# Kernel optimization log

Measured on AMD Instinct MI355X. Metric: run time of the kernel, lower is better.

Reference implementation:

```python
import jax, jax.numpy as jnp
import numpy as np

C = 1536          # interim_dim
D2 = 2 * C        # 3072, fc_nlb dim
LN_EPS = 1e-5


def setup_inputs() -> dict:
    key = jax.random.key(0)
    ks = jax.random.split(key, 24)
    B, L = 32, 1024
    s = 0.02
    inp = {
        "x": jax.random.normal(ks[0], (B, C), dtype=jnp.float32),
        "lfb_feats": jax.random.normal(ks[1], (B, L, C), dtype=jnp.float32),
        # 1x1 Conv1d weights act as (C_out, C_in) matmuls
        "theta_w": jax.random.normal(ks[2], (C, C), dtype=jnp.float32) * s,
        "theta_b": jnp.zeros((C,), dtype=jnp.float32),
        "phi_w": jax.random.normal(ks[3], (C, C), dtype=jnp.float32) * s,
        "phi_b": jnp.zeros((C,), dtype=jnp.float32),
        "gi_w": jax.random.normal(ks[4], (C, C), dtype=jnp.float32) * s,
        "gi_b": jnp.zeros((C,), dtype=jnp.float32),
        "ln_g": jnp.ones((C,), dtype=jnp.float32),
        "ln_b": jnp.zeros((C,), dtype=jnp.float32),
        "fc_w": jax.random.normal(ks[5], (C, C), dtype=jnp.float32) * s,
        "fc_b": jnp.zeros((C,), dtype=jnp.float32),
        "fc_nlb_w": jax.random.normal(ks[6], (D2, D2), dtype=jnp.float32) * s,
        "fc_nlb_b": jnp.zeros((D2,), dtype=jnp.float32),
        "fc1_w": jax.random.normal(ks[7], (1, 1024), dtype=jnp.float32) * s,
        "fc1_b": jnp.zeros((1,), dtype=jnp.float32),
        "fc2_w": jax.random.normal(ks[8], (1, 1024), dtype=jnp.float32) * s,
        "fc2_b": jnp.zeros((1,), dtype=jnp.float32),
        "fc3_w": jax.random.normal(ks[9], (1, 1024), dtype=jnp.float32) * s,
        "fc3_b": jnp.zeros((1,), dtype=jnp.float32),
        "fct_w": jax.random.normal(ks[10], (1, D2), dtype=jnp.float32) * s,
        "fct_b": jnp.zeros((1,), dtype=jnp.float32),
    }
    return inp


def _layernorm(x, g, b):
    mu = jnp.mean(x, axis=-1, keepdims=True)
    var = jnp.mean(jnp.square(x - mu), axis=-1, keepdims=True)
    return (x - mu) * jax.lax.rsqrt(var + LN_EPS) * g + b


def reference(x, lfb_feats, theta_w, theta_b, phi_w, phi_b, gi_w, gi_b,
              ln_g, ln_b, fc_w, fc_b, fc_nlb_w, fc_nlb_b,
              fc1_w, fc1_b, fc2_w, fc2_b, fc3_w, fc3_b, fct_w, fct_b):
    # --- _NLBlock on feats = x.unsqueeze(1): query sequence length is 1 ---
    # note: scale = 1/sqrt(1/C) = sqrt(C) (as in the original code)
    scale = jnp.sqrt(jnp.asarray(C, dtype=x.dtype))
    theta = x @ theta_w.T + theta_b                       # (B, C)
    phi = lfb_feats @ phi_w.T + phi_b                     # (B, L, C)
    gi = lfb_feats @ gi_w.T + gi_b                        # (B, L, C)
    scores = jnp.einsum('bc,blc->bl', theta, phi) * scale  # (B, L)
    attn = jax.nn.softmax(scores, axis=-1)
    o = jnp.einsum('bl,blc->bc', attn, gi)                # (B, C)
    o = jax.nn.relu(_layernorm(o, ln_g, ln_b))
    o = o @ fc_w.T + fc_b                                 # dropout -> identity (eval)
    longterm = o + x                                      # residual, (B, C)

    # --- head ---
    feats = jnp.concatenate([x, longterm], axis=1)        # (B, 2C)
    feats = jax.nn.relu(feats @ fc_nlb_w.T + fc_nlb_b)    # dropout -> identity
    f1 = feats[:, :1024]
    f2 = feats[:, 1024:2048]
    f3 = feats[:, 2048:3072]
    p1 = f1 @ fc1_w.T + fc1_b
    p2 = f2 @ fc2_w.T + fc2_b
    p3 = f3 @ fc3_w.T + fc3_b
    pt = feats @ fct_w.T + fct_b
    return jnp.concatenate([p1, p2, p3, pt], axis=1)      # (B, 4)
```

## Files before the change

kernel.cpp:

```cpp
#include <hip/hip_runtime.h>
#include <math.h>

#define B 32
#define C 1536
#define D2 3072
#define L 1024
#define KC 256
#define XPAD 260
#define CH 16
#define LPW 16

__device__ inline float dot4(float4 a, float4 b) {
    return a.x * b.x + a.y * b.y + a.z * b.z + a.w * b.w;
}

__global__ __launch_bounds__(256) void copy_x_k(const float* __restrict__ x,
                                                float* __restrict__ feats) {
    int i = blockIdx.x * 256 + threadIdx.x;
    int b = i / C, j = i % C;
    feats[b * D2 + j] = x[i];
}

__global__ __launch_bounds__(256) void transpose_k(const float* __restrict__ src,
                                                   float* __restrict__ dst, int n) {
    __shared__ float tile[32][33];
    int bx = blockIdx.x * 32, by = blockIdx.y * 32;
    int tx = threadIdx.x & 31, ty0 = threadIdx.x >> 5;
    #pragma unroll
    for (int r = 0; r < 4; ++r) {
        int ty = ty0 + r * 8;
        tile[ty][tx] = src[(size_t)(by + ty) * n + bx + tx];
    }
    __syncthreads();
    #pragma unroll
    for (int r = 0; r < 4; ++r) {
        int ty = ty0 + r * 8;
        dst[(size_t)(bx + ty) * n + by + tx] = tile[tx][ty];
    }
}

__global__ __launch_bounds__(256) void gemm32_splitk(const float* __restrict__ A,
                                                     const float* __restrict__ W,
                                                     float* __restrict__ part,
                                                     int N, int K) {
    __shared__ float xs[32 * XPAD];
    __shared__ float wsm[32 * XPAD];
    int tid = threadIdx.x;
    int j0 = blockIdx.x * 32;
    int kb = blockIdx.y;
    int k0 = kb * KC;

    #pragma unroll
    for (int r = 0; r < 8; ++r) {
        int f = tid + 256 * r;
        int b = f >> 6, kq = f & 63;
        float4 v = *(const float4*)(A + (size_t)b * K + k0 + 4 * kq);
        *(float4*)(xs + b * XPAD + 4 * kq) = v;
    }
    #pragma unroll
    for (int r = 0; r < 8; ++r) {
        int f = tid + 256 * r;
        int j = f >> 6, kq = f & 63;
        float4 v = *(const float4*)(W + (size_t)(j0 + j) * K + k0 + 4 * kq);
        *(float4*)(wsm + j * XPAD + 4 * kq) = v;
    }
    __syncthreads();

    int bb = (tid & 15) * 2;
    int jj = (tid >> 4) * 2;
    const float* x0 = xs + bb * XPAD;
    const float* x1 = xs + (bb + 1) * XPAD;
    const float* w0 = wsm + jj * XPAD;
    const float* w1 = wsm + (jj + 1) * XPAD;
    float a00 = 0.f, a01 = 0.f, a10 = 0.f, a11 = 0.f;
    #pragma unroll 8
    for (int k = 0; k < KC; k += 4) {
        float4 xa = *(const float4*)(x0 + k);
        float4 xb = *(const float4*)(x1 + k);
        float4 wa = *(const float4*)(w0 + k);
        float4 wb = *(const float4*)(w1 + k);
        a00 += dot4(xa, wa); a01 += dot4(xa, wb);
        a10 += dot4(xb, wa); a11 += dot4(xb, wb);
    }
    float* p = part + (size_t)kb * 32 * N;
    p[(size_t)bb * N + j0 + jj]           = a00;
    p[(size_t)bb * N + j0 + jj + 1]       = a01;
    p[(size_t)(bb + 1) * N + j0 + jj]     = a10;
    p[(size_t)(bb + 1) * N + j0 + jj + 1] = a11;
}

__global__ __launch_bounds__(256) void reduce_part(const float* __restrict__ part,
                                                   const float* __restrict__ bias,
                                                   const float* __restrict__ addx,
                                                   float* __restrict__ out,
                                                   float* __restrict__ feats,
                                                   int N, int ksplit, int mode) {
    int i = blockIdx.x * 256 + threadIdx.x;
    int b = i / N, j = i % N;
    float s = 0.f;
    for (int kk = 0; kk < ksplit; ++kk) s += part[(size_t)kk * 32 * N + i];
    if (bias) s += bias[j];
    if (mode == 2) {
        feats[(size_t)b * D2 + C + j] = s + addx[(size_t)b * C + j];
    } else if (mode == 3) {
        out[i] = fmaxf(s, 0.f);
    } else {
        out[i] = s;
    }
}

__global__ __launch_bounds__(256) void flash_k(const float* __restrict__ u,
                                               const float* __restrict__ lfb,
                                               float* __restrict__ pm,
                                               float* __restrict__ ps,
                                               float* __restrict__ pv) {
    int chunk = blockIdx.x;
    int b = blockIdx.y;
    int wave = threadIdx.x >> 6;
    int lane = threadIdx.x & 63;
    int widx = chunk * 4 + wave;

    const float scale = 39.19183588453085f;

    float uu[24];
    const float* ub = u + (size_t)b * C;
    #pragma unroll
    for (int t = 0; t < 6; ++t)
        *(float4*)(uu + 4 * t) = *(const float4*)(ub + 4 * lane + 256 * t);

    float m = -INFINITY, s = 0.f;
    float vv[24];
    #pragma unroll
    for (int t = 0; t < 24; ++t) vv[t] = 0.f;

    int l0 = chunk * (L / CH) + wave;
    for (int i = 0; i < LPW; ++i) {
        int l = l0 + i * 4;
        const float* row = lfb + ((size_t)b * L + l) * C;
        float xx[24];
        #pragma unroll
        for (int t = 0; t < 6; ++t)
            *(float4*)(xx + 4 * t) = *(const float4*)(row + 4 * lane + 256 * t);
        float d = 0.f;
        #pragma unroll
        for (int t = 0; t < 24; ++t) d += xx[t] * uu[t];
        #pragma unroll
        for (int off = 32; off > 0; off >>= 1) d += __shfl_xor(d, off, 64);
        float score = d * scale;
        float mn = fmaxf(m, score);
        float alpha = __expf(m - mn);
        float p = __expf(score - mn);
        s = s * alpha + p;
        #pragma unroll
        for (int t = 0; t < 24; ++t) vv[t] = vv[t] * alpha + p * xx[t];
        m = mn;
    }

    if (lane == 0) { pm[b * 64 + widx] = m; ps[b * 64 + widx] = s; }
    float* pvb = pv + ((size_t)b * 64 + widx) * C;
    #pragma unroll
    for (int t = 0; t < 6; ++t)
        *(float4*)(pvb + 4 * lane + 256 * t) = *(const float4*)(vv + 4 * t);
}

__global__ __launch_bounds__(256) void combine_k(const float* __restrict__ pm,
                                                 const float* __restrict__ ps,
                                                 const float* __restrict__ pv,
                                                 float* __restrict__ v) {
    int b = blockIdx.x;
    int tid = threadIdx.x;
    __shared__ float coef[64];
    if (tid < 64) {
        float mj = pm[b * 64 + tid];
        float M = mj;
        #pragma unroll
        for (int off = 32; off > 0; off >>= 1) M = fmaxf(M, __shfl_xor(M, off, 64));
        float ej = expf(mj - M);
        float S = ps[b * 64 + tid] * ej;
        #pragma unroll
        for (int off = 32; off > 0; off >>= 1) S += __shfl_xor(S, off, 64);
        coef[tid] = ej / S;
    }
    __syncthreads();
    for (int c = tid; c < C; c += 256) {
        float acc = 0.f;
        #pragma unroll 8
        for (int j = 0; j < 64; ++j)
            acc += coef[j] * pv[((size_t)b * 64 + j) * C + c];
        v[(size_t)b * C + c] = acc;
    }
}

__global__ __launch_bounds__(256) void ln_relu_k(const float* __restrict__ o,
                                                 const float* __restrict__ g,
                                                 const float* __restrict__ bt,
                                                 float* __restrict__ out) {
    int b = blockIdx.x, tid = threadIdx.x;
    __shared__ float r1[4], r2[4];
    const float* ob = o + (size_t)b * C;
    float lv[6];
    float s1 = 0.f, s2 = 0.f;
    #pragma unroll
    for (int t = 0; t < 6; ++t) {
        float x = ob[tid + 256 * t];
        lv[t] = x; s1 += x; s2 += x * x;
    }
    #pragma unroll
    for (int off = 32; off > 0; off >>= 1) {
        s1 += __shfl_xor(s1, off, 64);
        s2 += __shfl_xor(s2, off, 64);
    }
    int wave = tid >> 6, lane = tid & 63;
    if (lane == 0) { r1[wave] = s1; r2[wave] = s2; }
    __syncthreads();
    s1 = r1[0] + r1[1] + r1[2] + r1[3];
    s2 = r2[0] + r2[1] + r2[2] + r2[3];
    float mu = s1 / (float)C;
    float var = s2 / (float)C - mu * mu;
    float rstd = 1.0f / sqrtf(var + 1e-5f);
    #pragma unroll
    for (int t = 0; t < 6; ++t) {
        int c = tid + 256 * t;
        float y = (lv[t] - mu) * rstd * g[c] + bt[c];
        out[(size_t)b * C + c] = fmaxf(y, 0.f);
    }
}

__global__ __launch_bounds__(256) void heads_k(const float* __restrict__ h,
                                               const float* __restrict__ w1, const float* __restrict__ b1,
                                               const float* __restrict__ w2, const float* __restrict__ b2,
                                               const float* __restrict__ w3, const float* __restrict__ b3,
                                               const float* __restrict__ wt, const float* __restrict__ bt,
                                               float* __restrict__ out) {
    int b = blockIdx.x;
    int wave = threadIdx.x >> 6, lane = threadIdx.x & 63;
    const float* hb = h + (size_t)b * D2;
    float acc = 0.f;
    if (wave < 3) {
        const float* w = (wave == 0) ? w1 : ((wave == 1) ? w2 : w3);
        const float* hh = hb + wave * 1024;
        #pragma unroll
        for (int t = 0; t < 16; ++t) acc += hh[lane + 64 * t] * w[lane + 64 * t];
    } else {
        #pragma unroll
        for (int t = 0; t < 48; ++t) acc += hb[lane + 64 * t] * wt[lane + 64 * t];
    }
    #pragma unroll
    for (int off = 32; off > 0; off >>= 1) acc += __shfl_xor(acc, off, 64);
    if (lane == 0) {
        float bias = (wave == 0) ? b1[0] : (wave == 1) ? b2[0] : (wave == 2) ? b3[0] : bt[0];
        out[b * 4 + wave] = acc + bias;
    }
}

extern "C" void kernel_launch(void* const* d_in, const int* in_sizes, int n_in,
                              void* d_out, int out_size, void* d_ws, size_t ws_size,
                              hipStream_t stream) {
    (void)in_sizes; (void)n_in; (void)out_size; (void)ws_size;
    const float* x       = (const float*)d_in[0];
    const float* lfb     = (const float*)d_in[1];
    const float* theta_w = (const float*)d_in[2];
    const float* theta_b = (const float*)d_in[3];
    const float* phi_w   = (const float*)d_in[4];
    const float* gi_w    = (const float*)d_in[6];
    const float* gi_b    = (const float*)d_in[7];
    const float* ln_g    = (const float*)d_in[8];
    const float* ln_b    = (const float*)d_in[9];
    const float* fc_w    = (const float*)d_in[10];
    const float* fc_b    = (const float*)d_in[11];
    const float* fcn_w   = (const float*)d_in[12];
    const float* fcn_b   = (const float*)d_in[13];
    const float* w1 = (const float*)d_in[14]; const float* b1 = (const float*)d_in[15];
    const float* w2 = (const float*)d_in[16]; const float* b2 = (const float*)d_in[17];
    const float* w3 = (const float*)d_in[18]; const float* b3 = (const float*)d_in[19];
    const float* wt = (const float*)d_in[20]; const float* bt = (const float*)d_in[21];
    float* out = (float*)d_out;
    float* w = (float*)d_ws;

    float* theta = w;
    float* u     = w + 49152;
    float* part  = w + 98304;
    float* phiT  = w + 1277952;
    float* pm    = w + 98304;
    float* ps    = w + 100352;
    float* pv    = w + 102400;
    float* vbuf  = w + 3637248;
    float* obuf  = w + 3686400;
    float* oln   = w + 3735552;
    float* feats = w + 3784704;
    float* h     = w + 3883008;

    copy_x_k<<<192, 256, 0, stream>>>(x, feats);
    transpose_k<<<dim3(48, 48), 256, 0, stream>>>(phi_w, phiT, C);

    gemm32_splitk<<<dim3(48, 6), 256, 0, stream>>>(x, theta_w, part, C, C);
    reduce_part<<<192, 256, 0, stream>>>(part, theta_b, nullptr, theta, nullptr, C, 6, 0);

    gemm32_splitk<<<dim3(48, 6), 256, 0, stream>>>(theta, phiT, part, C, C);
    reduce_part<<<192, 256, 0, stream>>>(part, nullptr, nullptr, u, nullptr, C, 6, 0);

    flash_k<<<dim3(CH, B), 256, 0, stream>>>(u, lfb, pm, ps, pv);
    combine_k<<<B, 256, 0, stream>>>(pm, ps, pv, vbuf);

    gemm32_splitk<<<dim3(48, 6), 256, 0, stream>>>(vbuf, gi_w, part, C, C);
    reduce_part<<<192, 256, 0, stream>>>(part, gi_b, nullptr, obuf, nullptr, C, 6, 0);

    ln_relu_k<<<B, 256, 0, stream>>>(obuf, ln_g, ln_b, oln);

    gemm32_splitk<<<dim3(48, 6), 256, 0, stream>>>(oln, fc_w, part, C, C);
    reduce_part<<<192, 256, 0, stream>>>(part, fc_b, x, nullptr, feats, C, 6, 2);

    gemm32_splitk<<<dim3(96, 12), 256, 0, stream>>>(feats, fcn_w, part, D2, D2);
    reduce_part<<<384, 256, 0, stream>>>(part, fcn_b, nullptr, h, nullptr, D2, 12, 3);

    heads_k<<<B, 256, 0, stream>>>(h, w1, b1, w2, b2, w3, b3, wt, bt, out);
}
```

Before: 473.5 us.

## Retile skinny GEMMs with 4x4 register tiles, swizzled LDS, and fused reductions

Replaces the split-K GEMM with a 32x128 tile kernel that computes a 4x4 register tile per thread, stages K in chunks of 64 through XOR-swizzled shared memory, and loops over two K chunks per block. Grids and reduction split counts change to match. The x copy is folded into the residual reduce, the gi reduce is fused with LayerNorm/ReLU, and combine_k is split across column blocks for more parallelism. Together these aim to cut launch count, raise arithmetic intensity per LDS load, and improve occupancy for the memory-bound combine. The cost is more partial sums for the reduce kernels to read.

```diff
diff --git a/kernel.cpp b/kernel.cpp
--- a/kernel.cpp
+++ b/kernel.cpp
@@ -5,8 +5,8 @@
 #define C 1536
 #define D2 3072
 #define L 1024
-#define KC 256
-#define XPAD 260
+#define KC 64
+#define KQ 16
 #define CH 16
 #define LPW 16
 
@@ -14,11 +14,8 @@
     return a.x * b.x + a.y * b.y + a.z * b.z + a.w * b.w;
 }
 
-__global__ __launch_bounds__(256) void copy_x_k(const float* __restrict__ x,
-                                                float* __restrict__ feats) {
-    int i = blockIdx.x * 256 + threadIdx.x;
-    int b = i / C, j = i % C;
-    feats[b * D2 + j] = x[i];
+__device__ inline int sw(int row, int q) {
+    return row * KC + ((q ^ ((row >> 2) & 7)) << 2);
 }
 
 __global__ __launch_bounds__(256) void transpose_k(const float* __restrict__ src,
@@ -39,54 +36,61 @@
     }
 }
 
-__global__ __launch_bounds__(256) void gemm32_splitk(const float* __restrict__ A,
-                                                     const float* __restrict__ W,
-                                                     float* __restrict__ part,
-                                                     int N, int K) {
-    __shared__ float xs[32 * XPAD];
-    __shared__ float wsm[32 * XPAD];
+__global__ __launch_bounds__(256) void gemm32t4(const float* __restrict__ A,
+                                                const float* __restrict__ W,
+                                                float* __restrict__ part,
+                                                int N, int K, int kchunks) {
+    __shared__ float xs[32 * KC];
+    __shared__ float wsm[128 * KC];
     int tid = threadIdx.x;
-    int j0 = blockIdx.x * 32;
+    int j0 = blockIdx.x * 128;
     int kb = blockIdx.y;
-    int k0 = kb * KC;
-
-    #pragma unroll
-    for (int r = 0; r < 8; ++r) {
-        int f = tid + 256 * r;
-        int b = f >> 6, kq = f & 63;
-        float4 v = *(const float4*)(A + (size_t)b * K + k0 + 4 * kq);
-        *(float4*)(xs + b * XPAD + 4 * kq) = v;
-    }
-    #pragma unroll
-    for (int r = 0; r < 8; ++r) {
-        int f = tid + 256 * r;
-        int j = f >> 6, kq = f & 63;
-        float4 v = *(const float4*)(W + (size_t)(j0 + j) * K + k0 + 4 * kq);
-        *(float4*)(wsm + j * XPAD + 4 * kq) = v;
-    }
-    __syncthreads();
-
-    int bb = (tid & 15) * 2;
-    int jj = (tid >> 4) * 2;
-    const float* x0 = xs + bb * XPAD;
-    const float* x1 = xs + (bb + 1) * XPAD;
-    const float* w0 = wsm + jj * XPAD;
-    const float* w1 = wsm + (jj + 1) * XPAD;
-    float a00 = 0.f, a01 = 0.f, a10 = 0.f, a11 = 0.f;
-    #pragma unroll 8
-    for (int k = 0; k < KC; k += 4) {
-        float4 xa = *(const float4*)(x0 + k);
-        float4 xb = *(const float4*)(x1 + k);
-        float4 wa = *(const float4*)(w0 + k);
-        float4 wb = *(const float4*)(w1 + k);
-        a00 += dot4(xa, wa); a01 += dot4(xa, wb);
-        a10 += dot4(xb, wa); a11 += dot4(xb, wb);
-    }
-    float* p = part + (size_t)kb * 32 * N;
-    p[(size_t)bb * N + j0 + jj]           = a00;
-    p[(size_t)bb * N + j0 + jj + 1]       = a01;
-    p[(size_t)(bb + 1) * N + j0 + jj]     = a10;
-    p[(size_t)(bb + 1) * N + j0 + jj + 1] = a11;
+    int tb = tid & 7;
+    int tj = tid >> 3;
+
+    float4 acc[4];
+    #pragma unroll
+    for (int r = 0; r < 4; ++r) acc[r] = make_float4(0.f, 0.f, 0.f, 0.f);
+
+    for (int c = 0; c < kchunks; ++c) {
+        int k0 = (kb * kchunks + c) * KC;
+        __syncthreads();
+        #pragma unroll
+        for (int p = 0; p < 2; ++p) {
+            int f = tid + 256 * p;
+            int row = f >> 4, q = f & 15;
+            float4 v = *(const float4*)(A + (size_t)row * K + k0 + 4 * q);
+            *(float4*)(xs + sw(row, q)) = v;
+        }
+        #pragma unroll
+        for (int p = 0; p < 8; ++p) {
+            int f = tid + 256 * p;
+            int row = f >> 4, q = f & 15;
+            float4 v = *(const float4*)(W + (size_t)(j0 + row) * K + k0 + 4 * q);
+            *(float4*)(wsm + sw(row, q)) = v;
+        }
+        __syncthreads();
+        #pragma unroll
+        for (int kq = 0; kq < KQ; ++kq) {
+            float4 xq[4], wq[4];
+            #pragma unroll
+            for (int r = 0; r < 4; ++r) {
+                xq[r] = *(const float4*)(xs + sw(4 * tb + r, kq));
+                wq[r] = *(const float4*)(wsm + sw(4 * tj + r, kq));
+            }
+            #pragma unroll
+            for (int r = 0; r < 4; ++r) {
+                acc[r].x += dot4(xq[r], wq[0]);
+                acc[r].y += dot4(xq[r], wq[1]);
+                acc[r].z += dot4(xq[r], wq[2]);
+                acc[r].w += dot4(xq[r], wq[3]);
+            }
+        }
+    }
+    #pragma unroll
+    for (int r = 0; r < 4; ++r) {
+        *(float4*)(part + ((size_t)kb * 32 + 4 * tb + r) * N + j0 + 4 * tj) = acc[r];
+    }
 }
 
 __global__ __launch_bounds__(256) void reduce_part(const float* __restrict__ part,
@@ -98,14 +102,55 @@
     int i = blockIdx.x * 256 + threadIdx.x;
     int b = i / N, j = i % N;
     float s = 0.f;
-    for (int kk = 0; kk < ksplit; ++kk) s += part[(size_t)kk * 32 * N + i];
+    for (int kk = 0; kk < ksplit; ++kk) s += part[((size_t)kk * 32 + b) * N + j];
     if (bias) s += bias[j];
     if (mode == 2) {
-        feats[(size_t)b * D2 + C + j] = s + addx[(size_t)b * C + j];
+        float xv = addx[i];
+        feats[(size_t)b * D2 + j] = xv;
+        feats[(size_t)b * D2 + C + j] = s + xv;
     } else if (mode == 3) {
         out[i] = fmaxf(s, 0.f);
     } else {
         out[i] = s;
+    }
+}
+
+__global__ __launch_bounds__(256) void reduce_ln_relu(const float* __restrict__ part,
+                                                      const float* __restrict__ bias,
+                                                      const float* __restrict__ g,
+                                                      const float* __restrict__ bt,
+                                                      float* __restrict__ out,
+                                                      int ksplit) {
+    int b = blockIdx.x, tid = threadIdx.x;
+    __shared__ float r1[4], r2[4];
+    float lv[6];
+    float s1 = 0.f, s2 = 0.f;
+    #pragma unroll
+    for (int t = 0; t < 6; ++t) {
+        int c = tid + 256 * t;
+        float acc = 0.f;
+        for (int kk = 0; kk < ksplit; ++kk) acc += part[((size_t)kk * 32 + b) * C + c];
+        acc += bias[c];
+        lv[t] = acc; s1 += acc; s2 += acc * acc;
+    }
+    #pragma unroll
+    for (int off = 32; off > 0; off >>= 1) {
+        s1 += __shfl_xor(s1, off, 64);
+        s2 += __shfl_xor(s2, off, 64);
+    }
+    int wave = tid >> 6, lane = tid & 63;
+    if (lane == 0) { r1[wave] = s1; r2[wave] = s2; }
+    __syncthreads();
+    s1 = r1[0] + r1[1] + r1[2] + r1[3];
+    s2 = r2[0] + r2[1] + r2[2] + r2[3];
+    float mu = s1 / (float)C;
+    float var = s2 / (float)C - mu * mu;
+    float rstd = 1.0f / sqrtf(var + 1e-5f);
+    #pragma unroll
+    for (int t = 0; t < 6; ++t) {
+        int c = tid + 256 * t;
+        float y = (lv[t] - mu) * rstd * g[c] + bt[c];
+        out[(size_t)b * C + c] = fmaxf(y, 0.f);
     }
 }
 
@@ -167,7 +212,8 @@
                                                  const float* __restrict__ ps,
                                                  const float* __restrict__ pv,
                                                  float* __restrict__ v) {
-    int b = blockIdx.x;
+    int cc = blockIdx.x;
+    int b = blockIdx.y;
     int tid = threadIdx.x;
     __shared__ float coef[64];
     if (tid < 64) {
@@ -182,48 +228,12 @@
         coef[tid] = ej / S;
     }
     __syncthreads();
-    for (int c = tid; c < C; c += 256) {
-        float acc = 0.f;
-        #pragma unroll 8
-        for (int j = 0; j < 64; ++j)
-            acc += coef[j] * pv[((size_t)b * 64 + j) * C + c];
-        v[(size_t)b * C + c] = acc;
-    }
-}
-
-__global__ __launch_bounds__(256) void ln_relu_k(const float* __restrict__ o,
-                                                 const float* __restrict__ g,
-                                                 const float* __restrict__ bt,
-                                                 float* __restrict__ out) {
-    int b = blockIdx.x, tid = threadIdx.x;
-    __shared__ float r1[4], r2[4];
-    const float* ob = o + (size_t)b * C;
-    float lv[6];
-    float s1 = 0.f, s2 = 0.f;
-    #pragma unroll
-    for (int t = 0; t < 6; ++t) {
-        float x = ob[tid + 256 * t];
-        lv[t] = x; s1 += x; s2 += x * x;
-    }
-    #pragma unroll
-    for (int off = 32; off > 0; off >>= 1) {
-        s1 += __shfl_xor(s1, off, 64);
-        s2 += __shfl_xor(s2, off, 64);
-    }
-    int wave = tid >> 6, lane = tid & 63;
-    if (lane == 0) { r1[wave] = s1; r2[wave] = s2; }
-    __syncthreads();
-    s1 = r1[0] + r1[1] + r1[2] + r1[3];
-    s2 = r2[0] + r2[1] + r2[2] + r2[3];
-    float mu = s1 / (float)C;
-    float var = s2 / (float)C - mu * mu;
-    float rstd = 1.0f / sqrtf(var + 1e-5f);
-    #pragma unroll
-    for (int t = 0; t < 6; ++t) {
-        int c = tid + 256 * t;
-        float y = (lv[t] - mu) * rstd * g[c] + bt[c];
-        out[(size_t)b * C + c] = fmaxf(y, 0.f);
-    }
+    int c = cc * 256 + tid;
+    float acc = 0.f;
+    #pragma unroll 8
+    for (int j = 0; j < 64; ++j)
+        acc += coef[j] * pv[((size_t)b * 64 + j) * C + c];
+    v[(size_t)b * C + c] = acc;
 }
 
 __global__ __launch_bounds__(256) void heads_k(const float* __restrict__ h,
@@ -277,41 +287,37 @@
     float* out = (float*)d_out;
     float* w = (float*)d_ws;
 
-    float* theta = w;
-    float* u     = w + 49152;
-    float* part  = w + 98304;
-    float* phiT  = w + 1277952;
-    float* pm    = w + 98304;
-    float* ps    = w + 100352;
-    float* pv    = w + 102400;
-    float* vbuf  = w + 3637248;
-    float* obuf  = w + 3686400;
-    float* oln   = w + 3735552;
-    float* feats = w + 3784704;
-    float* h     = w + 3883008;
-
-    copy_x_k<<<192, 256, 0, stream>>>(x, feats);
+    float* phiT  = w;
+    float* part  = w + 2359296;
+    float* pv    = w + 4718592;
+    float* pm    = w + 7864320;
+    float* ps    = w + 7866368;
+    float* theta = w + 7868416;
+    float* u     = w + 7917568;
+    float* vbuf  = w + 7966720;
+    float* oln   = w + 8015872;
+    float* feats = w + 8065024;
+    float* h     = w + 8163328;
+
     transpose_k<<<dim3(48, 48), 256, 0, stream>>>(phi_w, phiT, C);
 
-    gemm32_splitk<<<dim3(48, 6), 256, 0, stream>>>(x, theta_w, part, C, C);
-    reduce_part<<<192, 256, 0, stream>>>(part, theta_b, nullptr, theta, nullptr, C, 6, 0);
-
-    gemm32_splitk<<<dim3(48, 6), 256, 0, stream>>>(theta, phiT, part, C, C);
-    reduce_part<<<192, 256, 0, stream>>>(part, nullptr, nullptr, u, nullptr, C, 6, 0);
+    gemm32t4<<<dim3(12, 12), 256, 0, stream>>>(x, theta_w, part, C, C, 2);
+    reduce_part<<<192, 256, 0, stream>>>(part, theta_b, nullptr, theta, nullptr, C, 12, 0);
+
+    gemm32t4<<<dim3(12, 12), 256, 0, stream>>>(theta, phiT, part, C, C, 2);
+    reduce_part<<<192, 256, 0, stream>>>(part, nullptr, nullptr, u, nullptr, C, 12, 0);
 
     flash_k<<<dim3(CH, B), 256, 0, stream>>>(u, lfb, pm, ps, pv);
-    combine_k<<<B, 256, 0, stream>>>(pm, ps, pv, vbuf);
-
-    gemm32_splitk<<<dim3(48, 6), 256, 0, stream>>>(vbuf, gi_w, part, C, C);
-    reduce_part<<<192, 256, 0, stream>>>(part, gi_b, nullptr, obuf, nullptr, C, 6, 0);
-
-    ln_relu_k<<<B, 256, 0, stream>>>(obuf, ln_g, ln_b, oln);
-
-    gemm32_splitk<<<dim3(48, 6), 256, 0, stream>>>(oln, fc_w, part, C, C);
-    reduce_part<<<192, 256, 0, stream>>>(part, fc_b, x, nullptr, feats, C, 6, 2);
-
-    gemm32_splitk<<<dim3(96, 12), 256, 0, stream>>>(feats, fcn_w, part, D2, D2);
-    reduce_part<<<384, 256, 0, stream>>>(part, fcn_b, nullptr, h, nullptr, D2, 12, 3);
+    combine_k<<<dim3(6, B), 256, 0, stream>>>(pm, ps, pv, vbuf);
+
+    gemm32t4<<<dim3(12, 12), 256, 0, stream>>>(vbuf, gi_w, part, C, C, 2);
+    reduce_ln_relu<<<B, 256, 0, stream>>>(part, gi_b, ln_g, ln_b, oln, 12);
+
+    gemm32t4<<<dim3(12, 12), 256, 0, stream>>>(oln, fc_w, part, C, C, 2);
+    reduce_part<<<192, 256, 0, stream>>>(part, fc_b, x, nullptr, feats, C, 12, 2);
+
+    gemm32t4<<<dim3(24, 24), 256, 0, stream>>>(feats, fcn_w, part, D2, D2, 2);
+    reduce_part<<<384, 256, 0, stream>>>(part, fcn_b, nullptr, h, nullptr, D2, 24, 3);
 
     heads_k<<<B, 256, 0, stream>>>(h, w1, b1, w2, b2, w3, b3, wt, bt, out);
 }
```

Result: slower. 525.2 us (+10.9%).
